# Kernel tuning notes

Hardware: AMD Instinct MI355X
Metric: run time of the kernel (lower is better)

## Reference

```python
import jax, jax.numpy as jnp
import numpy as np

N_NODES = 50000
N_PAIRS = 600000  # undirected pairs -> 1.2M directed edges
DIM = 64
STEPS = 4


def setup_inputs() -> dict:
    key = jax.random.key(0)
    ks = jax.random.split(key, 10)
    u = jax.random.randint(ks[0], (N_PAIRS,), 0, N_NODES, dtype=jnp.int32)
    v = jax.random.randint(ks[1], (N_PAIRS,), 0, N_NODES, dtype=jnp.int32)
    # interleave so edge 2i and 2i+1 are reverses of each other
    edge_src = jnp.stack([u, v], axis=1).reshape(-1)
    edge_dst = jnp.stack([v, u], axis=1).reshape(-1)
    E = 2 * N_PAIRS
    rev_index = (jnp.arange(E, dtype=jnp.int32) ^ 1)
    node_feature = jax.random.normal(ks[2], (N_NODES, DIM), dtype=jnp.float32)
    edge_feature = jax.random.normal(ks[3], (E, DIM), dtype=jnp.float32)
    s = 0.05
    W_init = jax.random.normal(ks[4], (2 * DIM, DIM), dtype=jnp.float32) * s
    b_init = jnp.zeros((DIM,), dtype=jnp.float32)
    W_steps = jax.random.normal(ks[5], (STEPS, DIM, DIM), dtype=jnp.float32) * s
    b_steps = jnp.zeros((STEPS, DIM), dtype=jnp.float32)
    W_proj = jax.random.normal(ks[6], (2 * DIM, DIM), dtype=jnp.float32) * s
    b_proj = jnp.zeros((DIM,), dtype=jnp.float32)
    return {
        'node_feature': node_feature, 'edge_feature': edge_feature,
        'edge_src': edge_src, 'edge_dst': edge_dst, 'rev_index': rev_index,
        'W_init': W_init, 'b_init': b_init,
        'W_steps': W_steps, 'b_steps': b_steps,
        'W_proj': W_proj, 'b_proj': b_proj,
    }


def reference(node_feature, edge_feature, edge_src, edge_dst, rev_index,
              W_init, b_init, W_steps, b_steps, W_proj, b_proj):
    N = node_feature.shape[0]
    # initial edge state: h0_e = relu(W_i [x_src(e) || e_feat])  [E, DIM]
    h0 = jax.nn.relu(
        jnp.concatenate([node_feature[edge_src], edge_feature], axis=-1) @ W_init + b_init)
    h = h0
    for t in range(W_steps.shape[0]):
        # scatter edge states to their destination node, gather back at edge source,
        # and exclude the reverse edge's state (directed message passing)
        agg = jax.ops.segment_sum(h, edge_dst, num_segments=N)  # [N, DIM]
        m = agg[edge_src] - h[rev_index]                         # [E, DIM]
        h = jax.nn.relu(h0 + m @ W_steps[t] + b_steps[t])
    # node readout: sum incoming directed edge states per node
    node_agg = jax.ops.segment_sum(h, edge_dst, num_segments=N)  # [N, DIM]
    node_out = jax.nn.relu(
        jnp.concatenate([node_feature, node_agg], axis=-1) @ W_proj + b_proj)
    return node_out, h
```

## Files before the change

kernel.cpp:

```cpp
#include <hip/hip_runtime.h>


#define DIM 64

__global__ __launch_bounds__(256) void k_init(
    const float* __restrict__ nf, const float* __restrict__ ef,
    const int* __restrict__ src,
    const float* __restrict__ W, const float* __restrict__ b,
    float* __restrict__ h0, float* __restrict__ h, int E) {
  __shared__ float Ws[128 * 64];
  __shared__ float bs[64];
  __shared__ float ins[4][128];
  const int tid = threadIdx.x;
  const int wave = tid >> 6, lane = tid & 63;
  for (int i = tid; i < 128 * 64; i += 256) Ws[i] = W[i];
  if (tid < 64) bs[tid] = b[tid];
  __syncthreads();
  const int stride = gridDim.x * 4;
  for (int base = blockIdx.x * 4; base < E; base += stride) {
    const int e = base + wave;
    const bool valid = (e < E);
    if (valid) {
      const int s = src[e];
      ins[wave][lane]      = nf[(size_t)s * DIM + lane];
      ins[wave][64 + lane] = ef[(size_t)e * DIM + lane];
    }
    __syncthreads();
    if (valid) {
      float acc = bs[lane];
      #pragma unroll
      for (int k = 0; k < 128; ++k)
        acc = fmaf(ins[wave][k], Ws[k * 64 + lane], acc);
      acc = fmaxf(acc, 0.0f);
      h0[(size_t)e * DIM + lane] = acc;
      h [(size_t)e * DIM + lane] = acc;
    }
    __syncthreads();
  }
}

__global__ __launch_bounds__(256) void k_scatter(
    const float* __restrict__ h, const int* __restrict__ dst,
    float* __restrict__ agg, int E) {
  size_t i = (size_t)blockIdx.x * blockDim.x + threadIdx.x;
  const size_t total = (size_t)E * DIM;
  const size_t stride = (size_t)gridDim.x * blockDim.x;
  for (; i < total; i += stride) {
    const int e = (int)(i >> 6);
    atomicAdd(&agg[(size_t)dst[e] * DIM + (i & 63)], h[i]);
  }
}

__global__ __launch_bounds__(256) void k_step(
    const float* __restrict__ agg, const int* __restrict__ src,
    const float* __restrict__ h0,
    const float* __restrict__ W, const float* __restrict__ b,
    float* __restrict__ h, int E) {
  __shared__ float Ws[64 * 64];
  __shared__ float bs[64];
  __shared__ float ins[4][2][64];
  const int tid = threadIdx.x;
  const int wave = tid >> 6, lane = tid & 63;
  for (int i = tid; i < 64 * 64; i += 256) Ws[i] = W[i];
  if (tid < 64) bs[tid] = b[tid];
  __syncthreads();
  const int P = E >> 1;
  const int stride = gridDim.x * 4;
  for (int base = blockIdx.x * 4; base < P; base += stride) {
    const int p = base + wave;
    const bool valid = (p < P);
    float hv0 = 0.f, hv1 = 0.f;
    if (valid) {
      const size_t e0 = (size_t)2 * p;
      hv0 = h[e0 * DIM + lane];
      hv1 = h[(e0 + 1) * DIM + lane];
      const int s0 = src[e0], s1 = src[e0 + 1];
      ins[wave][0][lane] = agg[(size_t)s0 * DIM + lane] - hv1;
      ins[wave][1][lane] = agg[(size_t)s1 * DIM + lane] - hv0;
    }
    __syncthreads();
    if (valid) {
      float acc0 = bs[lane], acc1 = bs[lane];
      #pragma unroll
      for (int k = 0; k < 64; ++k) {
        const float w = Ws[k * 64 + lane];
        acc0 = fmaf(ins[wave][0][k], w, acc0);
        acc1 = fmaf(ins[wave][1][k], w, acc1);
      }
      const size_t e0 = (size_t)2 * p;
      const float h00 = h0[e0 * DIM + lane];
      const float h01 = h0[(e0 + 1) * DIM + lane];
      h[e0 * DIM + lane]       = fmaxf(h00 + acc0, 0.0f);
      h[(e0 + 1) * DIM + lane] = fmaxf(h01 + acc1, 0.0f);
    }
    __syncthreads();
  }
}

__global__ __launch_bounds__(256) void k_readout(
    const float* __restrict__ nf, const float* __restrict__ agg,
    const float* __restrict__ W, const float* __restrict__ b,
    float* __restrict__ out, int N) {
  __shared__ float Ws[128 * 64];
  __shared__ float bs[64];
  __shared__ float ins[4][128];
  const int tid = threadIdx.x;
  const int wave = tid >> 6, lane = tid & 63;
  for (int i = tid; i < 128 * 64; i += 256) Ws[i] = W[i];
  if (tid < 64) bs[tid] = b[tid];
  __syncthreads();
  const int stride = gridDim.x * 4;
  for (int base = blockIdx.x * 4; base < N; base += stride) {
    const int n = base + wave;
    const bool valid = (n < N);
    if (valid) {
      ins[wave][lane]      = nf[(size_t)n * DIM + lane];
      ins[wave][64 + lane] = agg[(size_t)n * DIM + lane];
    }
    __syncthreads();
    if (valid) {
      float acc = bs[lane];
      #pragma unroll
      for (int k = 0; k < 128; ++k)
        acc = fmaf(ins[wave][k], Ws[k * 64 + lane], acc);
      out[(size_t)n * DIM + lane] = fmaxf(acc, 0.0f);
    }
    __syncthreads();
  }
}

extern "C" void kernel_launch(void* const* d_in, const int* in_sizes, int n_in,
                              void* d_out, int out_size, void* d_ws, size_t ws_size,
                              hipStream_t stream) {
  const float* nf     = (const float*)d_in[0];
  const float* ef     = (const float*)d_in[1];
  const int*   src    = (const int*)d_in[2];
  const int*   dst    = (const int*)d_in[3];
  const float* W_init = (const float*)d_in[5];
  const float* b_init = (const float*)d_in[6];
  const float* W_st   = (const float*)d_in[7];
  const float* b_st   = (const float*)d_in[8];
  const float* W_proj = (const float*)d_in[9];
  const float* b_proj = (const float*)d_in[10];

  const int N = in_sizes[0] / DIM;
  const int E = in_sizes[2];
  const int STEPS = in_sizes[7] / (DIM * DIM);

  float* node_out = (float*)d_out;
  float* h        = (float*)d_out + (size_t)N * DIM;
  float* agg      = (float*)d_ws;
  float* h0       = (float*)d_ws + (size_t)N * DIM;

  const int gInit = 1024, gStep = 2048, gScat = 4096, gRead = 1024;

  k_init<<<gInit, 256, 0, stream>>>(nf, ef, src, W_init, b_init, h0, h, E);
  for (int t = 0; t < STEPS; ++t) {
    hipMemsetAsync(agg, 0, (size_t)N * DIM * sizeof(float), stream);
    k_scatter<<<gScat, 256, 0, stream>>>(h, dst, agg, E);
    k_step<<<gStep, 256, 0, stream>>>(agg, src, h0,
                                      W_st + (size_t)t * DIM * DIM,
                                      b_st + (size_t)t * DIM, h, E);
  }
  hipMemsetAsync(agg, 0, (size_t)N * DIM * sizeof(float), stream);
  k_scatter<<<gScat, 256, 0, stream>>>(h, dst, agg, E);
  k_readout<<<gRead, 256, 0, stream>>>(nf, agg, W_proj, b_proj, node_out, N);
}
```

Measured before the change: 3.980 ms.

## Fuse scatter-add into init/step kernels with double-buffered aggregates and register weights

```diff
diff --git a/kernel.cpp b/kernel.cpp
--- a/kernel.cpp
+++ b/kernel.cpp
@@ -5,95 +5,113 @@
 
 __global__ __launch_bounds__(256) void k_init(
     const float* __restrict__ nf, const float* __restrict__ ef,
-    const int* __restrict__ src,
+    const int* __restrict__ src, const int* __restrict__ dst,
     const float* __restrict__ W, const float* __restrict__ b,
-    float* __restrict__ h0, float* __restrict__ h, int E) {
-  __shared__ float Ws[128 * 64];
-  __shared__ float bs[64];
-  __shared__ float ins[4][128];
-  const int tid = threadIdx.x;
-  const int wave = tid >> 6, lane = tid & 63;
-  for (int i = tid; i < 128 * 64; i += 256) Ws[i] = W[i];
-  if (tid < 64) bs[tid] = b[tid];
-  __syncthreads();
-  const int stride = gridDim.x * 4;
-  for (int base = blockIdx.x * 4; base < E; base += stride) {
-    const int e = base + wave;
-    const bool valid = (e < E);
-    if (valid) {
-      const int s = src[e];
-      ins[wave][lane]      = nf[(size_t)s * DIM + lane];
-      ins[wave][64 + lane] = ef[(size_t)e * DIM + lane];
-    }
-    __syncthreads();
-    if (valid) {
-      float acc = bs[lane];
-      #pragma unroll
-      for (int k = 0; k < 128; ++k)
-        acc = fmaf(ins[wave][k], Ws[k * 64 + lane], acc);
-      acc = fmaxf(acc, 0.0f);
-      h0[(size_t)e * DIM + lane] = acc;
-      h [(size_t)e * DIM + lane] = acc;
-    }
-    __syncthreads();
-  }
-}
-
-__global__ __launch_bounds__(256) void k_scatter(
-    const float* __restrict__ h, const int* __restrict__ dst,
-    float* __restrict__ agg, int E) {
-  size_t i = (size_t)blockIdx.x * blockDim.x + threadIdx.x;
-  const size_t total = (size_t)E * DIM;
-  const size_t stride = (size_t)gridDim.x * blockDim.x;
-  for (; i < total; i += stride) {
-    const int e = (int)(i >> 6);
-    atomicAdd(&agg[(size_t)dst[e] * DIM + (i & 63)], h[i]);
+    float* __restrict__ h0, float* __restrict__ aggA, int E) {
+  __shared__ float ins[4][4][2 * DIM];
+  const int tid = threadIdx.x, wave = tid >> 6, lane = tid & 63;
+  float wcol[128];
+  #pragma unroll
+  for (int k = 0; k < 128; ++k) wcol[k] = W[k * 64 + lane];
+  const float bl = b[lane];
+  for (int base = blockIdx.x * 16 + wave * 4; base < E; base += gridDim.x * 16) {
+    int dArr[4];
+    #pragma unroll
+    for (int j = 0; j < 4; ++j) {
+      const int e = base + j;
+      if (e < E) {
+        const int s = src[e];
+        dArr[j] = dst[e];
+        ins[wave][j][lane]       = nf[(size_t)s * DIM + lane];
+        ins[wave][j][DIM + lane] = ef[(size_t)e * DIM + lane];
+      }
+    }
+    float acc[4] = {bl, bl, bl, bl};
+    const float4* q0 = (const float4*)ins[wave][0];
+    const float4* q1 = (const float4*)ins[wave][1];
+    const float4* q2 = (const float4*)ins[wave][2];
+    const float4* q3 = (const float4*)ins[wave][3];
+    #pragma unroll
+    for (int k4 = 0; k4 < 32; ++k4) {
+      const float4 i0 = q0[k4], i1 = q1[k4], i2 = q2[k4], i3 = q3[k4];
+      const float w0 = wcol[4*k4], w1 = wcol[4*k4+1], w2 = wcol[4*k4+2], w3 = wcol[4*k4+3];
+      acc[0] = fmaf(i0.x, w0, acc[0]); acc[1] = fmaf(i1.x, w0, acc[1]);
+      acc[2] = fmaf(i2.x, w0, acc[2]); acc[3] = fmaf(i3.x, w0, acc[3]);
+      acc[0] = fmaf(i0.y, w1, acc[0]); acc[1] = fmaf(i1.y, w1, acc[1]);
+      acc[2] = fmaf(i2.y, w1, acc[2]); acc[3] = fmaf(i3.y, w1, acc[3]);
+      acc[0] = fmaf(i0.z, w2, acc[0]); acc[1] = fmaf(i1.z, w2, acc[1]);
+      acc[2] = fmaf(i2.z, w2, acc[2]); acc[3] = fmaf(i3.z, w2, acc[3]);
+      acc[0] = fmaf(i0.w, w3, acc[0]); acc[1] = fmaf(i1.w, w3, acc[1]);
+      acc[2] = fmaf(i2.w, w3, acc[2]); acc[3] = fmaf(i3.w, w3, acc[3]);
+    }
+    #pragma unroll
+    for (int j = 0; j < 4; ++j) {
+      const int e = base + j;
+      if (e < E) {
+        const float v = fmaxf(acc[j], 0.0f);
+        h0[(size_t)e * DIM + lane] = v;
+        atomicAdd(&aggA[(size_t)dArr[j] * DIM + lane], v);
+      }
+    }
   }
 }
 
 __global__ __launch_bounds__(256) void k_step(
     const float* __restrict__ agg, const int* __restrict__ src,
-    const float* __restrict__ h0,
-    const float* __restrict__ W, const float* __restrict__ b,
-    float* __restrict__ h, int E) {
-  __shared__ float Ws[64 * 64];
-  __shared__ float bs[64];
-  __shared__ float ins[4][2][64];
-  const int tid = threadIdx.x;
-  const int wave = tid >> 6, lane = tid & 63;
-  for (int i = tid; i < 64 * 64; i += 256) Ws[i] = W[i];
-  if (tid < 64) bs[tid] = b[tid];
-  __syncthreads();
+    const float* __restrict__ h0, const float* __restrict__ W, const float* __restrict__ b,
+    const float* __restrict__ hin, float* __restrict__ hout,
+    float* __restrict__ aggN, int E) {
+  __shared__ float ins[4][8][DIM];
+  const int tid = threadIdx.x, wave = tid >> 6, lane = tid & 63;
+  float wcol[64];
+  #pragma unroll
+  for (int k = 0; k < 64; ++k) wcol[k] = W[k * 64 + lane];
+  const float bl = b[lane];
   const int P = E >> 1;
-  const int stride = gridDim.x * 4;
-  for (int base = blockIdx.x * 4; base < P; base += stride) {
-    const int p = base + wave;
-    const bool valid = (p < P);
-    float hv0 = 0.f, hv1 = 0.f;
-    if (valid) {
-      const size_t e0 = (size_t)2 * p;
-      hv0 = h[e0 * DIM + lane];
-      hv1 = h[(e0 + 1) * DIM + lane];
-      const int s0 = src[e0], s1 = src[e0 + 1];
-      ins[wave][0][lane] = agg[(size_t)s0 * DIM + lane] - hv1;
-      ins[wave][1][lane] = agg[(size_t)s1 * DIM + lane] - hv0;
-    }
-    __syncthreads();
-    if (valid) {
-      float acc0 = bs[lane], acc1 = bs[lane];
-      #pragma unroll
-      for (int k = 0; k < 64; ++k) {
-        const float w = Ws[k * 64 + lane];
-        acc0 = fmaf(ins[wave][0][k], w, acc0);
-        acc1 = fmaf(ins[wave][1][k], w, acc1);
-      }
-      const size_t e0 = (size_t)2 * p;
-      const float h00 = h0[e0 * DIM + lane];
-      const float h01 = h0[(e0 + 1) * DIM + lane];
-      h[e0 * DIM + lane]       = fmaxf(h00 + acc0, 0.0f);
-      h[(e0 + 1) * DIM + lane] = fmaxf(h01 + acc1, 0.0f);
-    }
-    __syncthreads();
+  for (int base = blockIdx.x * 16 + wave * 4; base < P; base += gridDim.x * 16) {
+    int s0a[4], s1a[4];
+    #pragma unroll
+    for (int j = 0; j < 4; ++j) {
+      const int p = base + j;
+      if (p < P) {
+        const size_t e0 = (size_t)2 * p;
+        const int s0 = src[e0], s1 = src[e0 + 1];
+        s0a[j] = s0; s1a[j] = s1;
+        const float hv0 = hin[e0 * DIM + lane];
+        const float hv1 = hin[e0 * DIM + DIM + lane];
+        ins[wave][2*j][lane]     = agg[(size_t)s0 * DIM + lane] - hv1;
+        ins[wave][2*j + 1][lane] = agg[(size_t)s1 * DIM + lane] - hv0;
+      }
+    }
+    float acc[8] = {bl, bl, bl, bl, bl, bl, bl, bl};
+    #pragma unroll
+    for (int k4 = 0; k4 < 16; ++k4) {
+      float4 iq[8];
+      #pragma unroll
+      for (int e = 0; e < 8; ++e) iq[e] = ((const float4*)ins[wave][e])[k4];
+      const float w0 = wcol[4*k4], w1 = wcol[4*k4+1], w2 = wcol[4*k4+2], w3 = wcol[4*k4+3];
+      #pragma unroll
+      for (int e = 0; e < 8; ++e) acc[e] = fmaf(iq[e].x, w0, acc[e]);
+      #pragma unroll
+      for (int e = 0; e < 8; ++e) acc[e] = fmaf(iq[e].y, w1, acc[e]);
+      #pragma unroll
+      for (int e = 0; e < 8; ++e) acc[e] = fmaf(iq[e].z, w2, acc[e]);
+      #pragma unroll
+      for (int e = 0; e < 8; ++e) acc[e] = fmaf(iq[e].w, w3, acc[e]);
+    }
+    #pragma unroll
+    for (int j = 0; j < 4; ++j) {
+      const int p = base + j;
+      if (p < P) {
+        const size_t e0 = (size_t)2 * p;
+        const float v0 = fmaxf(h0[e0 * DIM + lane] + acc[2*j], 0.0f);
+        const float v1 = fmaxf(h0[e0 * DIM + DIM + lane] + acc[2*j + 1], 0.0f);
+        hout[e0 * DIM + lane]       = v0;
+        hout[e0 * DIM + DIM + lane] = v1;
+        atomicAdd(&aggN[(size_t)s1a[j] * DIM + lane], v0);
+        atomicAdd(&aggN[(size_t)s0a[j] * DIM + lane], v1);
+      }
+    }
   }
 }
 
@@ -101,31 +119,44 @@
     const float* __restrict__ nf, const float* __restrict__ agg,
     const float* __restrict__ W, const float* __restrict__ b,
     float* __restrict__ out, int N) {
-  __shared__ float Ws[128 * 64];
-  __shared__ float bs[64];
-  __shared__ float ins[4][128];
-  const int tid = threadIdx.x;
-  const int wave = tid >> 6, lane = tid & 63;
-  for (int i = tid; i < 128 * 64; i += 256) Ws[i] = W[i];
-  if (tid < 64) bs[tid] = b[tid];
-  __syncthreads();
-  const int stride = gridDim.x * 4;
-  for (int base = blockIdx.x * 4; base < N; base += stride) {
-    const int n = base + wave;
-    const bool valid = (n < N);
-    if (valid) {
-      ins[wave][lane]      = nf[(size_t)n * DIM + lane];
-      ins[wave][64 + lane] = agg[(size_t)n * DIM + lane];
-    }
-    __syncthreads();
-    if (valid) {
-      float acc = bs[lane];
-      #pragma unroll
-      for (int k = 0; k < 128; ++k)
-        acc = fmaf(ins[wave][k], Ws[k * 64 + lane], acc);
-      out[(size_t)n * DIM + lane] = fmaxf(acc, 0.0f);
-    }
-    __syncthreads();
+  __shared__ float ins[4][4][2 * DIM];
+  const int tid = threadIdx.x, wave = tid >> 6, lane = tid & 63;
+  float wcol[128];
+  #pragma unroll
+  for (int k = 0; k < 128; ++k) wcol[k] = W[k * 64 + lane];
+  const float bl = b[lane];
+  for (int base = blockIdx.x * 16 + wave * 4; base < N; base += gridDim.x * 16) {
+    #pragma unroll
+    for (int j = 0; j < 4; ++j) {
+      const int n = base + j;
+      if (n < N) {
+        ins[wave][j][lane]       = nf[(size_t)n * DIM + lane];
+        ins[wave][j][DIM + lane] = agg[(size_t)n * DIM + lane];
+      }
+    }
+    float acc[4] = {bl, bl, bl, bl};
+    const float4* q0 = (const float4*)ins[wave][0];
+    const float4* q1 = (const float4*)ins[wave][1];
+    const float4* q2 = (const float4*)ins[wave][2];
+    const float4* q3 = (const float4*)ins[wave][3];
+    #pragma unroll
+    for (int k4 = 0; k4 < 32; ++k4) {
+      const float4 i0 = q0[k4], i1 = q1[k4], i2 = q2[k4], i3 = q3[k4];
+      const float w0 = wcol[4*k4], w1 = wcol[4*k4+1], w2 = wcol[4*k4+2], w3 = wcol[4*k4+3];
+      acc[0] = fmaf(i0.x, w0, acc[0]); acc[1] = fmaf(i1.x, w0, acc[1]);
+      acc[2] = fmaf(i2.x, w0, acc[2]); acc[3] = fmaf(i3.x, w0, acc[3]);
+      acc[0] = fmaf(i0.y, w1, acc[0]); acc[1] = fmaf(i1.y, w1, acc[1]);
+      acc[2] = fmaf(i2.y, w1, acc[2]); acc[3] = fmaf(i3.y, w1, acc[3]);
+      acc[0] = fmaf(i0.z, w2, acc[0]); acc[1] = fmaf(i1.z, w2, acc[1]);
+      acc[2] = fmaf(i2.z, w2, acc[2]); acc[3] = fmaf(i3.z, w2, acc[3]);
+      acc[0] = fmaf(i0.w, w3, acc[0]); acc[1] = fmaf(i1.w, w3, acc[1]);
+      acc[2] = fmaf(i2.w, w3, acc[2]); acc[3] = fmaf(i3.w, w3, acc[3]);
+    }
+    #pragma unroll
+    for (int j = 0; j < 4; ++j) {
+      const int n = base + j;
+      if (n < N) out[(size_t)n * DIM + lane] = fmaxf(acc[j], 0.0f);
+    }
   }
 }
 
@@ -149,20 +180,26 @@
 
   float* node_out = (float*)d_out;
   float* h        = (float*)d_out + (size_t)N * DIM;
-  float* agg      = (float*)d_ws;
-  float* h0       = (float*)d_ws + (size_t)N * DIM;
-
-  const int gInit = 1024, gStep = 2048, gScat = 4096, gRead = 1024;
-
-  k_init<<<gInit, 256, 0, stream>>>(nf, ef, src, W_init, b_init, h0, h, E);
+  float* aggA     = (float*)d_ws;
+  float* aggB     = (float*)d_ws + (size_t)N * DIM;
+  float* h0       = (float*)d_ws + (size_t)2 * N * DIM;
+
+  const size_t aggBytes = (size_t)N * DIM * sizeof(float);
+
+  hipMemsetAsync(aggA, 0, aggBytes, stream);
+  hipMemsetAsync(aggB, 0, aggBytes, stream);
+  k_init<<<2048, 256, 0, stream>>>(nf, ef, src, dst, W_init, b_init, h0, aggA, E);
+
+  float* rd = aggA;
+  float* wr = aggB;
   for (int t = 0; t < STEPS; ++t) {
-    hipMemsetAsync(agg, 0, (size_t)N * DIM * sizeof(float), stream);
-    k_scatter<<<gScat, 256, 0, stream>>>(h, dst, agg, E);
-    k_step<<<gStep, 256, 0, stream>>>(agg, src, h0,
-                                      W_st + (size_t)t * DIM * DIM,
-                                      b_st + (size_t)t * DIM, h, E);
-  }
-  hipMemsetAsync(agg, 0, (size_t)N * DIM * sizeof(float), stream);
-  k_scatter<<<gScat, 256, 0, stream>>>(h, dst, agg, E);
-  k_readout<<<gRead, 256, 0, stream>>>(nf, agg, W_proj, b_proj, node_out, N);
-}
+    if (t > 0) hipMemsetAsync(wr, 0, aggBytes, stream);
+    const float* hin = (t == 0) ? h0 : h;
+    k_step<<<2048, 256, 0, stream>>>(rd, src, h0,
+                                     W_st + (size_t)t * DIM * DIM,
+                                     b_st + (size_t)t * DIM,
+                                     hin, h, wr, E);
+    float* tmp = rd; rd = wr; wr = tmp;
+  }
+  k_readout<<<1024, 256, 0, stream>>>(nf, rd, W_proj, b_proj, node_out, N);
+}
```

After: 5.590 ms. 1.4x slower.
